# Kernel optimization log

Measured on AMD Instinct MI355X. Metric: run time of the kernel, lower is better.

## Reference

```python
import jax, jax.numpy as jnp
import numpy as np

TEMPS = (0.02, 0.05, 0.2)
EPS = 1e-06


def _pairwise_dist_sq(x, y):
    # (N, M) squared L2 distances, clamped at 0 like the torch version
    dsq = (x * x).sum(-1)[:, None] + (y * y).sum(-1)[None, :] - 2.0 * (x @ y.T)
    return jnp.maximum(dsq, 0.0)


def reference(gen_features, pos_features, drift_scales):
    gen, pos = gen_features, pos_features
    N = gen.shape[0]
    # Distances are temperature-independent; compute once and reuse across temps.
    d_att = jnp.sqrt(_pairwise_dist_sq(gen, pos))  # (N_gen, N_pos)
    eye = jnp.eye(N, dtype=bool)
    dsq_rep = _pairwise_dist_sq(gen, gen)
    # diagonal gets masked to -inf in the logits anyway; replace 0 before sqrt for numerical safety
    d_rep = jnp.sqrt(jnp.where(eye, 1.0, dsq_rep))  # (N_gen, N_gen)

    drift_sum = jnp.zeros_like(gen)
    for i, T in enumerate(TEMPS):
        # attraction: sum_j softmax(-d/T)_ij * (pos_j - gen_i) == softmax @ pos - gen
        # (weights sum to 1 along axis=1, so the -gen_i term factors out)
        w_att = jax.nn.softmax(-d_att / T, axis=1)
        attraction = w_att @ pos - gen
        # repulsion: self-pair excluded via -inf logit (masked_fill(inf) on distances)
        logits_rep = jnp.where(eye, -jnp.inf, -d_rep / T)
        w_rep = jax.nn.softmax(logits_rep, axis=1)
        repulsion = w_rep @ gen - gen
        scale = jnp.maximum(drift_scales[i], EPS)
        drift_sum = drift_sum + (attraction - repulsion) / scale
    return drift_sum / len(TEMPS)


def setup_inputs() -> dict:
    key = jax.random.key(0)
    k1, k2 = jax.random.split(key)
    return {
        "gen_features": jax.random.normal(k1, (8192, 1024), dtype=jnp.float32),
        "pos_features": jax.random.normal(k2, (8192, 1024), dtype=jnp.float32),
        "drift_scales": jnp.ones((3,), dtype=jnp.float32),
    }
```

## Files before the change

kernel.cpp:

```cpp
#include <hip/hip_runtime.h>
#include <hip/hip_bf16.h>

#define NN 8192
#define DD 1024
#define KK 16384

using half8 = __attribute__((ext_vector_type(8))) _Float16;
using half4 = __attribute__((ext_vector_type(4))) _Float16;
using f32x4 = __attribute__((ext_vector_type(4))) float;
using u32x4 = __attribute__((ext_vector_type(4))) unsigned int;

__device__ __align__(16) _Float16 g_gh[(size_t)NN * DD];
__device__ __align__(16) _Float16 g_ph[(size_t)NN * DD];
__device__ __align__(16) _Float16 g_vt[(size_t)DD * KK];
__device__ float g_gn[NN];
__device__ float g_pn[NN];
__device__ __align__(16) unsigned short g_datt[(size_t)NN * NN];
__device__ __align__(16) unsigned short g_drep[(size_t)NN * NN];
__device__ __align__(16) _Float16 g_w[(size_t)NN * KK];
__device__ float g_part[2 * (size_t)NN * DD];

typedef const __attribute__((address_space(1))) void GV;
typedef __attribute__((address_space(3))) void LV;
__device__ inline void gload16(const void* g, void* l) {
    __builtin_amdgcn_global_load_lds((GV*)g, (LV*)l, 16, 0, 0);
}

__global__ __launch_bounds__(256) void k_conv(const float* __restrict__ gen,
                                              const float* __restrict__ pos) {
    int b = blockIdx.x;
    int r = b & (NN - 1);
    const float* src = (b < NN) ? gen : pos;
    _Float16* dsth = (b < NN) ? g_gh : g_ph;
    float* dstn = (b < NN) ? g_gn : g_pn;
    int t = threadIdx.x;
    const float4* s4 = (const float4*)(src + (size_t)r * DD);
    float4 x = s4[t];
    half4 h = {(_Float16)x.x, (_Float16)x.y, (_Float16)x.z, (_Float16)x.w};
    *(half4*)(dsth + (size_t)r * DD + t * 4) = h;
    float s = x.x * x.x + x.y * x.y + x.z * x.z + x.w * x.w;
#pragma unroll
    for (int off = 32; off; off >>= 1) s += __shfl_xor(s, off);
    __shared__ float red[4];
    if ((t & 63) == 0) red[t >> 6] = s;
    __syncthreads();
    if (t == 0) dstn[r] = red[0] + red[1] + red[2] + red[3];
}

__global__ __launch_bounds__(256) void k_tr(const float* __restrict__ pos,
                                            const float* __restrict__ gen) {
    int jt = blockIdx.x;
    int dt = blockIdx.y;
    int z = blockIdx.z;
    const float* src = z ? gen : pos;
    size_t cbase = z ? (size_t)NN : 0;
    __shared__ _Float16 tile[64][68];
    int t = threadIdx.x;
    int j0 = jt * 64, d0 = dt * 64;
#pragma unroll
    for (int p = 0; p < 4; p++) {
        int idx = t + p * 256;
        int r = idx >> 4;
        int c4 = idx & 15;
        float4 x = *(const float4*)(src + (size_t)(j0 + r) * DD + d0 + c4 * 4);
        tile[r][c4 * 4 + 0] = (_Float16)x.x;
        tile[r][c4 * 4 + 1] = (_Float16)x.y;
        tile[r][c4 * 4 + 2] = (_Float16)x.z;
        tile[r][c4 * 4 + 3] = (_Float16)x.w;
    }
    __syncthreads();
#pragma unroll
    for (int p = 0; p < 4; p++) {
        int idx = t + p * 256;
        int d = idx >> 4;
        int j4 = idx & 15;
        half4 h = {tile[j4 * 4 + 0][d], tile[j4 * 4 + 1][d],
                   tile[j4 * 4 + 2][d], tile[j4 * 4 + 3][d]};
        *(half4*)(g_vt + (size_t)(d0 + d) * KK + cbase + j0 + j4 * 4) = h;
    }
}

#define MFMA16(A_, B_, C_) __builtin_amdgcn_mfma_f32_16x16x32_f16(A_, B_, C_, 0, 0, 0)
#define BAR() __builtin_amdgcn_s_barrier()
#define LGKM0() do { asm volatile("s_waitcnt lgkmcnt(0)" ::: "memory"); \
                     __builtin_amdgcn_sched_barrier(0); } while (0)
#define VM4() asm volatile("s_waitcnt vmcnt(4)" ::: "memory")
#define VM0() asm volatile("s_waitcnt vmcnt(0)" ::: "memory")

__global__ __launch_bounds__(256, 3) void k_qk3() {
    __shared__ _Float16 sA[128 * 64];
    __shared__ _Float16 sB[128 * 64];
    int id = blockIdx.y * 64 + blockIdx.x;
    id = (id & 7) * 512 + (id >> 3);
    int rt = id >> 6, ct = id & 63;
    int rep = blockIdx.z;
    const _Float16* A = g_gh;
    const _Float16* B = rep ? g_gh : g_ph;
    const float* An = g_gn;
    const float* Bn = rep ? g_gn : g_pn;
    unsigned short* outp = rep ? g_drep : g_datt;

    int t = threadIdx.x;
    int w = t >> 6, lane = t & 63;
    int wm = w >> 1, wn = w & 1;
    int q = lane >> 4, li = lane & 15;

    int offA_[4][2], offB_[4][2];
#pragma unroll
    for (int m = 0; m < 4; ++m) {
        int rowa = wm * 64 + m * 16 + li;
        int rowb = wn * 64 + m * 16 + li;
#pragma unroll
        for (int kk = 0; kk < 2; ++kk) {
            offA_[m][kk] = rowa * 64 + ((kk * 4 + q) ^ (rowa & 7)) * 8;
            offB_[m][kk] = rowb * 64 + ((kk * 4 + q) ^ (rowb & 7)) * 8;
        }
    }

    int srow = t >> 3, sc = t & 7;
    int csrc = sc ^ (srow & 7);
    const _Float16* gA = A + (size_t)(rt * 128 + srow) * DD + csrc * 8;
    const _Float16* gB = B + (size_t)(ct * 128 + srow) * DD + csrc * 8;
    _Float16* dA = sA + t * 8;
    _Float16* dB = sB + t * 8;

    f32x4 acc[4][4] = {};
    for (int kt = 0; kt < DD / 64; ++kt) {
#pragma unroll
        for (int r = 0; r < 4; ++r) {
            gload16(gA + (size_t)(r * 32) * DD + kt * 64, dA + r * 2048);
            gload16(gB + (size_t)(r * 32) * DD + kt * 64, dB + r * 2048);
        }
        __syncthreads();
#pragma unroll
        for (int kk = 0; kk < 2; ++kk) {
            half8 a[4], b[4];
#pragma unroll
            for (int m = 0; m < 4; ++m) a[m] = *(const half8*)(sA + offA_[m][kk]);
#pragma unroll
            for (int n = 0; n < 4; ++n) b[n] = *(const half8*)(sB + offB_[n][kk]);
#pragma unroll
            for (int m = 0; m < 4; ++m)
#pragma unroll
                for (int n = 0; n < 4; ++n)
                    acc[m][n] = MFMA16(a[m], b[n], acc[m][n]);
        }
        __syncthreads();
    }

    unsigned short* sd = (unsigned short*)sA;
    float bnv[4];
#pragma unroll
    for (int n = 0; n < 4; ++n) bnv[n] = Bn[ct * 128 + wn * 64 + n * 16 + li];
#pragma unroll
    for (int m = 0; m < 4; ++m) {
#pragma unroll
        for (int r = 0; r < 4; ++r) {
            int row = wm * 64 + m * 16 + q * 4 + r;
            float an = An[rt * 128 + row];
#pragma unroll
            for (int n = 0; n < 4; ++n) {
                int col = wn * 64 + n * 16 + li;
                float dsq = an + bnv[n] - 2.0f * acc[m][n][r];
                float d = sqrtf(fmaxf(dsq, 0.0f));
                if (rep && (rt * 128 + row) == (ct * 128 + col)) d = 1e30f;
                float dv = fminf(d * 1024.0f + 0.5f, 65535.0f);
                sd[row * 128 + col] = (unsigned short)(int)dv;
            }
        }
    }
    __syncthreads();
    const u32x4* s4 = (const u32x4*)sd;
    int row16 = t >> 4, chunk = t & 15;
#pragma unroll
    for (int i = 0; i < 8; ++i) {
        int lrow = i * 16 + row16;
        u32x4 v = s4[lrow * 16 + chunk];
        u32x4* gp = (u32x4*)(outp + (size_t)(rt * 128 + lrow) * NN + ct * 128) + chunk;
        __builtin_nontemporal_store(v, gp);
    }
}

template <int LDK>
__device__ inline void gemm_core(const _Float16* __restrict__ A,
                                 const _Float16* __restrict__ B,
                                 int arow0, int brow0, int kcol0, int ntiles,
                                 _Float16* lds, f32x4 acc[8][4]) {
    int t = threadIdx.x;
    int w = t >> 6, lane = t & 63;
    int wm = w >> 2, wn = w & 3;
    int q = lane >> 4, li = lane & 15;
    _Float16* sA = lds;
    _Float16* sB = lds + 4 * 8192;

    int offA[8], offB[4];
#pragma unroll
    for (int m = 0; m < 8; ++m) {
        int row = wm * 128 + m * 16 + li;
        offA[m] = row * 32 + (q ^ ((row >> 1) & 3)) * 8;
    }
#pragma unroll
    for (int n = 0; n < 4; ++n) {
        int row = wn * 64 + n * 16 + li;
        offB[n] = row * 32 + (q ^ ((row >> 1) & 3)) * 8;
    }

    int rbase = w * 16 + (lane >> 2);
    int csrc = (lane & 3) ^ ((rbase >> 1) & 3);
    const _Float16* gA0 = A + (size_t)(arow0 + rbase) * LDK + kcol0 + csrc * 8;
    const _Float16* gA1 = gA0 + (size_t)128 * LDK;
    const _Float16* gB0 = B + (size_t)(brow0 + rbase) * LDK + kcol0 + csrc * 8;
    const _Float16* gB1 = gB0 + (size_t)128 * LDK;
    int ldst = w * 512;

#define STAGE_A(tile_) do { \
    gload16(gA0 + (size_t)(tile_) * 32, sA + ((tile_) & 3) * 8192 + ldst); \
    gload16(gA1 + (size_t)(tile_) * 32, sA + ((tile_) & 3) * 8192 + 4096 + ldst); } while (0)
#define STAGE_B(tile_) do { \
    gload16(gB0 + (size_t)(tile_) * 32, sB + ((tile_) & 3) * 8192 + ldst); \
    gload16(gB1 + (size_t)(tile_) * 32, sB + ((tile_) & 3) * 8192 + 4096 + ldst); } while (0)

    STAGE_A(0); STAGE_B(0); STAGE_A(1); STAGE_B(1);
    VM4();
    BAR();

    int nwin = ntiles >> 1;
    half8 af[4], bf[4], af2[4];
#pragma unroll 2
    for (int wi = 0; wi < nwin; ++wi) {
        int t0 = 2 * wi, t1 = t0 + 1;
        const _Float16* a0 = sA + (t0 & 3) * 8192;
        const _Float16* b0 = sB + (t0 & 3) * 8192;
        const _Float16* a1 = sA + (t1 & 3) * 8192;
        const _Float16* b1 = sB + (t1 & 3) * 8192;
#pragma unroll
        for (int m = 0; m < 4; ++m) af[m] = *(const half8*)(a0 + offA[m]);
#pragma unroll
        for (int n = 0; n < 4; ++n) bf[n] = *(const half8*)(b0 + offB[n]);
        if (t0 + 2 < ntiles) STAGE_A(t0 + 2);
        BAR();
        LGKM0();
        __builtin_amdgcn_s_setprio(1);
#pragma unroll
        for (int m = 0; m < 4; ++m)
#pragma unroll
            for (int n = 0; n < 4; ++n)
                acc[m][n] = MFMA16(af[m], bf[n], acc[m][n]);
        __builtin_amdgcn_s_setprio(0);
        BAR();
#pragma unroll
        for (int m = 0; m < 4; ++m) af2[m] = *(const half8*)(a0 + offA[m + 4]);
        if (t0 + 2 < ntiles) STAGE_B(t0 + 2);
        BAR();
        LGKM0();
        __builtin_amdgcn_s_setprio(1);
#pragma unroll
        for (int m = 0; m < 4; ++m)
#pragma unroll
            for (int n = 0; n < 4; ++n)
                acc[m + 4][n] = MFMA16(af2[m], bf[n], acc[m + 4][n]);
        __builtin_amdgcn_s_setprio(0);
        if (wi < nwin - 1) VM4(); else VM0();
        BAR();
#pragma unroll
        for (int m = 0; m < 4; ++m) af[m] = *(const half8*)(a1 + offA[m]);
#pragma unroll
        for (int n = 0; n < 4; ++n) bf[n] = *(const half8*)(b1 + offB[n]);
        if (t1 + 2 < ntiles) STAGE_A(t1 + 2);
        BAR();
        LGKM0();
        __builtin_amdgcn_s_setprio(1);
#pragma unroll
        for (int m = 0; m < 4; ++m)
#pragma unroll
            for (int n = 0; n < 4; ++n)
                acc[m][n] = MFMA16(af[m], bf[n], acc[m][n]);
        __builtin_amdgcn_s_setprio(0);
        BAR();
#pragma unroll
        for (int m = 0; m < 4; ++m) af2[m] = *(const half8*)(a1 + offA[m + 4]);
        if (t1 + 2 < ntiles) STAGE_B(t1 + 2);
        BAR();
        LGKM0();
        __builtin_amdgcn_s_setprio(1);
#pragma unroll
        for (int m = 0; m < 4; ++m)
#pragma unroll
            for (int n = 0; n < 4; ++n)
                acc[m + 4][n] = MFMA16(af2[m], bf[n], acc[m + 4][n]);
        __builtin_amdgcn_s_setprio(0);
        if (wi < nwin - 1) {
            VM4();
            BAR();
        }
    }
#undef STAGE_A
#undef STAGE_B
}

__global__ __launch_bounds__(256) void k_sw(const float* __restrict__ scales) {
    int i = blockIdx.x, t = threadIdx.x;
    const u32x4* ra = (const u32x4*)(g_datt + (size_t)i * NN);
    const u32x4* rr = (const u32x4*)(g_drep + (size_t)i * NN);
    float va[32], vr[32];
    float mna = 1e30f, mnr = 1e30f;
    const float SC = 1.0f / 1024.0f;
#pragma unroll
    for (int p = 0; p < 4; ++p) {
        u32x4 x = __builtin_nontemporal_load(&ra[t + p * 256]);
        u32x4 y = __builtin_nontemporal_load(&rr[t + p * 256]);
#pragma unroll
        for (int u = 0; u < 4; ++u) {
            float a0 = (float)(x[u] & 0xFFFFu) * SC;
            float a1 = (float)(x[u] >> 16) * SC;
            float r0 = (float)(y[u] & 0xFFFFu) * SC;
            float r1 = (float)(y[u] >> 16) * SC;
            va[p * 8 + u * 2 + 0] = a0; va[p * 8 + u * 2 + 1] = a1;
            vr[p * 8 + u * 2 + 0] = r0; vr[p * 8 + u * 2 + 1] = r1;
            mna = fminf(mna, fminf(a0, a1));
            mnr = fminf(mnr, fminf(r0, r1));
        }
    }
#pragma unroll
    for (int off = 32; off; off >>= 1) {
        mna = fminf(mna, __shfl_xor(mna, off));
        mnr = fminf(mnr, __shfl_xor(mnr, off));
    }
    __shared__ float sm[2][4];
    __shared__ float ss[6][4];
    int wv = t >> 6;
    if ((t & 63) == 0) { sm[0][wv] = mna; sm[1][wv] = mnr; }
    __syncthreads();
    mna = fminf(fminf(sm[0][0], sm[0][1]), fminf(sm[0][2], sm[0][3]));
    mnr = fminf(fminf(sm[1][0], sm[1][1]), fminf(sm[1][2], sm[1][3]));
    float s0 = 0.f, s1 = 0.f, s2 = 0.f, s3 = 0.f, s4 = 0.f, s5 = 0.f;
#pragma unroll
    for (int k = 0; k < 32; ++k) {
        float da = va[k] - mna;
        s0 += __expf(da * -50.0f); s1 += __expf(da * -20.0f); s2 += __expf(da * -5.0f);
        float dr = vr[k] - mnr;
        s3 += __expf(dr * -50.0f); s4 += __expf(dr * -20.0f); s5 += __expf(dr * -5.0f);
    }
#pragma unroll
    for (int off = 32; off; off >>= 1) {
        s0 += __shfl_xor(s0, off); s1 += __shfl_xor(s1, off); s2 += __shfl_xor(s2, off);
        s3 += __shfl_xor(s3, off); s4 += __shfl_xor(s4, off); s5 += __shfl_xor(s5, off);
    }
    if ((t & 63) == 0) {
        ss[0][wv] = s0; ss[1][wv] = s1; ss[2][wv] = s2;
        ss[3][wv] = s3; ss[4][wv] = s4; ss[5][wv] = s5;
    }
    __syncthreads();
    float l0 = ss[0][0] + ss[0][1] + ss[0][2] + ss[0][3];
    float l1 = ss[1][0] + ss[1][1] + ss[1][2] + ss[1][3];
    float l2 = ss[2][0] + ss[2][1] + ss[2][2] + ss[2][3];
    float l3 = ss[3][0] + ss[3][1] + ss[3][2] + ss[3][3];
    float l4 = ss[4][0] + ss[4][1] + ss[4][2] + ss[4][3];
    float l5 = ss[5][0] + ss[5][1] + ss[5][2] + ss[5][3];
    float i0 = 1.0f / (3.0f * fmaxf(scales[0], 1e-6f));
    float i1 = 1.0f / (3.0f * fmaxf(scales[1], 1e-6f));
    float i2 = 1.0f / (3.0f * fmaxf(scales[2], 1e-6f));
    float ca0 = i0 / l0, ca1 = i1 / l1, ca2 = i2 / l2;
    float cr0 = -i0 / l3, cr1 = -i1 / l4, cr2 = -i2 / l5;
    _Float16* wa = g_w + (size_t)i * KK;
    _Float16* wr = wa + NN;
#pragma unroll
    for (int p = 0; p < 4; ++p) {
        union { half8 h; u32x4 u; } ha, hr;
#pragma unroll
        for (int qq = 0; qq < 8; ++qq) {
            float da = va[p * 8 + qq] - mna;
            ha.h[qq] = (_Float16)(ca0 * __expf(da * -50.0f) + ca1 * __expf(da * -20.0f) +
                                  ca2 * __expf(da * -5.0f));
            float dr = vr[p * 8 + qq] - mnr;
            hr.h[qq] = (_Float16)(cr0 * __expf(dr * -50.0f) + cr1 * __expf(dr * -20.0f) +
                                  cr2 * __expf(dr * -5.0f));
        }
        __builtin_nontemporal_store(ha.u, (u32x4*)(wa + (size_t)(t + p * 256) * 8));
        __builtin_nontemporal_store(hr.u, (u32x4*)(wr + (size_t)(t + p * 256) * 8));
    }
}

__global__ __launch_bounds__(512, 2) void k_gemm2() {
    extern __shared__ _Float16 lds[];
    int id = blockIdx.y * 4 + blockIdx.x;
    id = (id & 7) * 16 + (id >> 3);
    int rt = id >> 2, ct = id & 3;
    int z = blockIdx.z;
    f32x4 acc[8][4] = {};
    gemm_core<KK>(g_w, g_vt, rt * 256, ct * 256, z * (KK / 2), (KK / 2) / 32, lds, acc);
    float* outp = g_part + (size_t)z * NN * DD;
    int t = threadIdx.x, w = t >> 6, lane = t & 63;
    int wm = w >> 2, wn = w & 3, q = lane >> 4, li = lane & 15;
#pragma unroll
    for (int m = 0; m < 8; ++m) {
#pragma unroll
        for (int r = 0; r < 4; ++r) {
            int gi = rt * 256 + wm * 128 + m * 16 + q * 4 + r;
            float* orow = outp + (size_t)gi * DD;
#pragma unroll
            for (int n = 0; n < 4; ++n) {
                int gj = ct * 256 + wn * 64 + n * 16 + li;
                orow[gj] = acc[m][n][r];
            }
        }
    }
}

__global__ __launch_bounds__(256) void k_red(float* __restrict__ out) {
    size_t base = (size_t)blockIdx.x * 256 + threadIdx.x;
    const float4* p0 = (const float4*)g_part;
    const float4* p1 = (const float4*)(g_part + (size_t)NN * DD);
    float4* o4 = (float4*)out;
#pragma unroll
    for (int p = 0; p < 4; ++p) {
        size_t idx = base + (size_t)p * 524288;
        float4 a = p0[idx], b = p1[idx];
        float4 c = {a.x + b.x, a.y + b.y, a.z + b.z, a.w + b.w};
        o4[idx] = c;
    }
}

extern "C" void kernel_launch(void* const* d_in, const int* in_sizes, int n_in,
                              void* d_out, int out_size, void* d_ws, size_t ws_size,
                              hipStream_t stream) {
    (void)in_sizes; (void)n_in; (void)d_ws; (void)ws_size; (void)out_size;
    const float* gen = (const float*)d_in[0];
    const float* pos = (const float*)d_in[1];
    const float* scales = (const float*)d_in[2];

    (void)hipFuncSetAttribute((const void*)k_gemm2, hipFuncAttributeMaxDynamicSharedMemorySize, 131072);

    k_conv<<<dim3(2 * NN), 256, 0, stream>>>(gen, pos);
    k_tr<<<dim3(128, 16, 2), 256, 0, stream>>>(pos, gen);
    k_qk3<<<dim3(64, 64, 2), 256, 0, stream>>>();
    k_sw<<<dim3(NN), 256, 0, stream>>>(scales);
    k_gemm2<<<dim3(4, 32, 2), 512, 131072, stream>>>();
    k_red<<<dim3(2048), 256, 0, stream>>>((float*)d_out);
}
```

Before: 913.6 us.

## Restructure distance GEMM into per-wave double-buffered pipeline without block barriers

The distance GEMM kernel now gives each wave its own private LDS region. Each wave loads only its own A/B rows in 32-wide k slices into a two-stage buffer. It waits on vmcnt instead of block-wide syncthreads, issues the next prefetch before its MFMAs, and raises wave priority around the MFMA block. This removes barrier stalls and overlaps global loads with compute. In exchange it uses more LDS, since each wave loads redundant A/B rows, and lowers the occupancy bound from 3 to 2 blocks. Separately, the nontemporal loads and stores on the distance and weight buffers become ordinary accesses, which could change how those buffers are cached between kernels.

```diff
diff --git a/kernel.cpp b/kernel.cpp
--- a/kernel.cpp
+++ b/kernel.cpp
@@ -85,11 +85,11 @@
 #define LGKM0() do { asm volatile("s_waitcnt lgkmcnt(0)" ::: "memory"); \
                      __builtin_amdgcn_sched_barrier(0); } while (0)
 #define VM4() asm volatile("s_waitcnt vmcnt(4)" ::: "memory")
+#define VM8() asm volatile("s_waitcnt vmcnt(8)" ::: "memory")
 #define VM0() asm volatile("s_waitcnt vmcnt(0)" ::: "memory")
 
-__global__ __launch_bounds__(256, 3) void k_qk3() {
-    __shared__ _Float16 sA[128 * 64];
-    __shared__ _Float16 sB[128 * 64];
+__global__ __launch_bounds__(256, 2) void k_qk7() {
+    __shared__ _Float16 lds[4 * 8192];
     int id = blockIdx.y * 64 + blockIdx.x;
     id = (id & 7) * 512 + (id >> 3);
     int rt = id >> 6, ct = id & 63;
@@ -100,55 +100,67 @@
     const float* Bn = rep ? g_gn : g_pn;
     unsigned short* outp = rep ? g_drep : g_datt;
 
-    int t = threadIdx.x;
-    int w = t >> 6, lane = t & 63;
+    int t = threadIdx.x, w = t >> 6, lane = t & 63;
     int wm = w >> 1, wn = w & 1;
     int q = lane >> 4, li = lane & 15;
-
-    int offA_[4][2], offB_[4][2];
+    int wbase = w * 8192;
+
+    int offA[4], offB[4];
 #pragma unroll
     for (int m = 0; m < 4; ++m) {
-        int rowa = wm * 64 + m * 16 + li;
-        int rowb = wn * 64 + m * 16 + li;
-#pragma unroll
-        for (int kk = 0; kk < 2; ++kk) {
-            offA_[m][kk] = rowa * 64 + ((kk * 4 + q) ^ (rowa & 7)) * 8;
-            offB_[m][kk] = rowb * 64 + ((kk * 4 + q) ^ (rowb & 7)) * 8;
-        }
-    }
-
-    int srow = t >> 3, sc = t & 7;
-    int csrc = sc ^ (srow & 7);
-    const _Float16* gA = A + (size_t)(rt * 128 + srow) * DD + csrc * 8;
-    const _Float16* gB = B + (size_t)(ct * 128 + srow) * DD + csrc * 8;
-    _Float16* dA = sA + t * 8;
-    _Float16* dB = sB + t * 8;
+        int row = m * 16 + li;
+        offA[m] = row * 32 + ((q ^ ((row >> 1) & 3)) * 8);
+    }
+#pragma unroll
+    for (int n = 0; n < 4; ++n) {
+        int row = n * 16 + li;
+        offB[n] = 2048 + row * 32 + ((q ^ ((row >> 1) & 3)) * 8);
+    }
+
+    int srow = lane >> 2, sc = lane & 3;
+    int csrc = sc ^ ((srow >> 1) & 3);
+    const _Float16* gA = A + (size_t)(rt * 128 + wm * 64 + srow) * DD + csrc * 8;
+    const _Float16* gB = B + (size_t)(ct * 128 + wn * 64 + srow) * DD + csrc * 8;
+
+#define STAGE7(s_) do { \
+    int sl_ = wbase + ((s_) & 1) * 4096; \
+    const _Float16* a_ = gA + (size_t)(s_) * 32; \
+    const _Float16* b_ = gB + (size_t)(s_) * 32; \
+    _Float16* dA_ = lds + sl_ + lane * 8; \
+    _Float16* dB_ = lds + sl_ + 2048 + lane * 8; \
+    gload16(a_, dA_);                         gload16(b_, dB_); \
+    gload16(a_ + (size_t)16 * DD, dA_ + 512); gload16(b_ + (size_t)16 * DD, dB_ + 512); \
+    gload16(a_ + (size_t)32 * DD, dA_ + 1024); gload16(b_ + (size_t)32 * DD, dB_ + 1024); \
+    gload16(a_ + (size_t)48 * DD, dA_ + 1536); gload16(b_ + (size_t)48 * DD, dB_ + 1536); \
+} while (0)
 
     f32x4 acc[4][4] = {};
-    for (int kt = 0; kt < DD / 64; ++kt) {
-#pragma unroll
-        for (int r = 0; r < 4; ++r) {
-            gload16(gA + (size_t)(r * 32) * DD + kt * 64, dA + r * 2048);
-            gload16(gB + (size_t)(r * 32) * DD + kt * 64, dB + r * 2048);
-        }
-        __syncthreads();
-#pragma unroll
-        for (int kk = 0; kk < 2; ++kk) {
-            half8 a[4], b[4];
-#pragma unroll
-            for (int m = 0; m < 4; ++m) a[m] = *(const half8*)(sA + offA_[m][kk]);
-#pragma unroll
-            for (int n = 0; n < 4; ++n) b[n] = *(const half8*)(sB + offB_[n][kk]);
-#pragma unroll
-            for (int m = 0; m < 4; ++m)
-#pragma unroll
-                for (int n = 0; n < 4; ++n)
-                    acc[m][n] = MFMA16(a[m], b[n], acc[m][n]);
-        }
-        __syncthreads();
-    }
-
-    unsigned short* sd = (unsigned short*)sA;
+    STAGE7(0); STAGE7(1);
+    VM8();
+
+    for (int kt = 0; kt < 32; ++kt) {
+        const _Float16* s = lds + wbase + (kt & 1) * 4096;
+        half8 a[4], b[4];
+#pragma unroll
+        for (int m = 0; m < 4; ++m) a[m] = *(const half8*)(s + offA[m]);
+#pragma unroll
+        for (int n = 0; n < 4; ++n) b[n] = *(const half8*)(s + offB[n]);
+        LGKM0();
+        if (kt + 2 < 32) STAGE7(kt + 2);
+        __builtin_amdgcn_s_setprio(1);
+#pragma unroll
+        for (int m = 0; m < 4; ++m)
+#pragma unroll
+            for (int n = 0; n < 4; ++n)
+                acc[m][n] = MFMA16(a[m], b[n], acc[m][n]);
+        __builtin_amdgcn_s_setprio(0);
+        if (kt < 31) {
+            if (kt + 2 < 32) VM8(); else VM0();
+        }
+    }
+
+    __syncthreads();
+    unsigned short* sd = (unsigned short*)lds;
     float bnv[4];
 #pragma unroll
     for (int n = 0; n < 4; ++n) bnv[n] = Bn[ct * 128 + wn * 64 + n * 16 + li];
@@ -171,13 +183,12 @@
     }
     __syncthreads();
     const u32x4* s4 = (const u32x4*)sd;
-    int row16 = t >> 4, chunk = t & 15;
 #pragma unroll
     for (int i = 0; i < 8; ++i) {
-        int lrow = i * 16 + row16;
-        u32x4 v = s4[lrow * 16 + chunk];
-        u32x4* gp = (u32x4*)(outp + (size_t)(rt * 128 + lrow) * NN + ct * 128) + chunk;
-        __builtin_nontemporal_store(v, gp);
+        int idx = i * 256 + t;
+        int row = idx >> 4, ch = idx & 15;
+        u32x4 v = s4[idx];
+        *((u32x4*)(outp + (size_t)(rt * 128 + row) * NN + ct * 128) + ch) = v;
     }
 }
 
@@ -307,8 +318,8 @@
     const float SC = 1.0f / 1024.0f;
 #pragma unroll
     for (int p = 0; p < 4; ++p) {
-        u32x4 x = __builtin_nontemporal_load(&ra[t + p * 256]);
-        u32x4 y = __builtin_nontemporal_load(&rr[t + p * 256]);
+        u32x4 x = ra[t + p * 256];
+        u32x4 y = rr[t + p * 256];
 #pragma unroll
         for (int u = 0; u < 4; ++u) {
             float a0 = (float)(x[u] & 0xFFFFu) * SC;
@@ -376,8 +387,8 @@
             hr.h[qq] = (_Float16)(cr0 * __expf(dr * -50.0f) + cr1 * __expf(dr * -20.0f) +
                                   cr2 * __expf(dr * -5.0f));
         }
-        __builtin_nontemporal_store(ha.u, (u32x4*)(wa + (size_t)(t + p * 256) * 8));
-        __builtin_nontemporal_store(hr.u, (u32x4*)(wr + (size_t)(t + p * 256) * 8));
+        *(u32x4*)(wa + (size_t)(t + p * 256) * 8) = ha.u;
+        *(u32x4*)(wr + (size_t)(t + p * 256) * 8) = hr.u;
     }
 }
 
@@ -433,7 +444,7 @@
 
     k_conv<<<dim3(2 * NN), 256, 0, stream>>>(gen, pos);
     k_tr<<<dim3(128, 16, 2), 256, 0, stream>>>(pos, gen);
-    k_qk3<<<dim3(64, 64, 2), 256, 0, stream>>>();
+    k_qk7<<<dim3(64, 64, 2), 256, 0, stream>>>();
     k_sw<<<dim3(NN), 256, 0, stream>>>(scales);
     k_gemm2<<<dim3(4, 32, 2), 512, 131072, stream>>>();
     k_red<<<dim3(2048), 256, 0, stream>>>((float*)d_out);
```

Result: slower. 1.181 ms (+29.3%).
